# Performance work log

Measured on AMD Instinct MI355X. Metric: run time of the kernel, lower is better.

## Reference

```python
import jax, jax.numpy as jnp
import numpy as np

D_MODEL = 512
EPS = 1e-5


def setup_inputs() -> dict:
    key = jax.random.key(0)
    k1, k2, k3 = jax.random.split(key, 3)
    B, N, D = 8, 2048, D_MODEL
    output = jax.random.normal(k1, (B, N, D), dtype=jnp.float32)
    # multiplicative 0/1 float mask over the [B, N, N] score matrix
    slf_attn_mask = jax.random.randint(k2, (B, N, N), 0, 2).astype(jnp.float32)
    # nn.Linear(d_model, d_model): weight [out, in], xavier-uniform; bias zeros-ish
    limit = float(np.sqrt(6.0 / (D + D)))
    W = jax.random.uniform(k3, (D, D), dtype=jnp.float32, minval=-limit, maxval=limit)
    b = jnp.zeros((D,), dtype=jnp.float32)
    return {"output": output, "slf_attn_mask": slf_attn_mask, "W": W, "b": b}


def reference(output, slf_attn_mask, W, b):
    temperature = jnp.asarray(D_MODEL, output.dtype) ** 0.5
    # scores: [B, N, N] = (q / temp) @ k^T, then multiplicative mask
    attn = jnp.einsum("bnd,bmd->bnm", output / temperature, output) * slf_attn_mask
    # F.normalize(p=2, dim=-1, eps=1e-5): x / max(||x||_2, eps)
    norm = jnp.sqrt(jnp.sum(attn * attn, axis=-1, keepdims=True))
    attn = attn / jnp.maximum(norm, EPS)
    # values: elu(Linear(output)), Linear uses W @ x + b with W [out, in]
    v = jax.nn.elu(jnp.einsum("bnd,ed->bne", output, W) + b)
    return jnp.einsum("bnm,bme->bne", attn, v)
```

## Files before the change

### kernel.cpp

```cpp
#include <hip/hip_runtime.h>
#include <hip/hip_bf16.h>

#define NSEQ 2048
#define DM 512
#define BATCH 8
#define GTOT (BATCH * NSEQ)
#define INV_T 0.044194173824159216f
#define EPSN 1e-5f

typedef __bf16 bf16_t;
typedef bf16_t bf16x8 __attribute__((ext_vector_type(8)));
typedef float f32x4 __attribute__((ext_vector_type(4)));
typedef unsigned short u16;
typedef unsigned int u32;

__device__ __forceinline__ u16 f2bf(float f) {
    u32 u = __builtin_bit_cast(u32, f);
    u32 r = (u + 0x7FFFu + ((u >> 16) & 1u)) >> 16;
    return (u16)r;
}

__global__ __launch_bounds__(256) void k_convert(
    const float* __restrict__ X, const float* __restrict__ W,
    u16* __restrict__ Kbf, u16* __restrict__ Wbf) {
    const long NK = (long)GTOT * DM / 4;
    const long NW = (long)DM * DM / 4;
    long i = (long)blockIdx.x * 256 + threadIdx.x;
    if (i < NK) {
        float4 f = ((const float4*)X)[i];
        ushort4 o;
        o.x = f2bf(f.x); o.y = f2bf(f.y); o.z = f2bf(f.z); o.w = f2bf(f.w);
        ((ushort4*)Kbf)[i] = o;
    } else if (i < NK + NW) {
        long j = i - NK;
        float4 f = ((const float4*)W)[j];
        ushort4 o;
        o.x = f2bf(f.x); o.y = f2bf(f.y); o.z = f2bf(f.z); o.w = f2bf(f.w);
        ((ushort4*)Wbf)[j] = o;
    }
}

__global__ __launch_bounds__(256, 2) void k_vgemm(
    const u16* __restrict__ Wbf, const u16* __restrict__ Kbf,
    const float* __restrict__ bias, u16* __restrict__ vT) {
    __shared__ __attribute__((aligned(16))) u16 Ks[32 * 520];
    const int tid = threadIdx.x;
    const int wave = tid >> 6, lane = tid & 63, quad = lane >> 4, l15 = lane & 15;
    const int etile = blockIdx.x & 7;
    const int mblk = blockIdx.x >> 3;
    const int ebase = etile * 64 + wave * 16;

    bf16x8 wf[16];
    {
        const u16* wp = Wbf + (long)(ebase + l15) * DM + quad * 8;
#pragma unroll
        for (int ks = 0; ks < 16; ++ks) wf[ks] = *(const bf16x8*)(wp + ks * 32);
    }
    float bvals[4];
#pragma unroll
    for (int r = 0; r < 4; ++r) bvals[r] = bias[ebase + quad * 4 + r];

    bf16x8 kreg[8];
    {
        const int g0 = mblk * 256;
#pragma unroll
        for (int j = 0; j < 8; ++j) {
            int c = tid + 256 * j;
            int row = c >> 6, col = c & 63;
            kreg[j] = *(const bf16x8*)(Kbf + (long)(g0 + row) * DM + col * 8);
        }
    }
    for (int mt = 0; mt < 8; ++mt) {
        const int g0 = mblk * 256 + mt * 32;
        __syncthreads();
#pragma unroll
        for (int j = 0; j < 8; ++j) {
            int c = tid + 256 * j;
            int row = c >> 6, col = c & 63;
            *(bf16x8*)(&Ks[row * 520 + col * 8]) = kreg[j];
        }
        __syncthreads();
        {
            int mtn = (mt + 1 < 8) ? mt + 1 : 0;
            const int gn = mblk * 256 + mtn * 32;
#pragma unroll
            for (int j = 0; j < 8; ++j) {
                int c = tid + 256 * j;
                int row = c >> 6, col = c & 63;
                kreg[j] = *(const bf16x8*)(Kbf + (long)(gn + row) * DM + col * 8);
            }
        }
        f32x4 acc[2] = {{0.f, 0.f, 0.f, 0.f}, {0.f, 0.f, 0.f, 0.f}};
#pragma unroll
        for (int ks = 0; ks < 16; ++ks) {
#pragma unroll
            for (int nt = 0; nt < 2; ++nt) {
                bf16x8 kf = *(const bf16x8*)(&Ks[(nt * 16 + l15) * 520 + ks * 32 + quad * 8]);
                acc[nt] = __builtin_amdgcn_mfma_f32_16x16x32_bf16(wf[ks], kf, acc[nt], 0, 0, 0);
            }
        }
#pragma unroll
        for (int nt = 0; nt < 2; ++nt) {
#pragma unroll
            for (int r = 0; r < 4; ++r) {
                int e = ebase + quad * 4 + r;
                int g = g0 + nt * 16 + l15;
                float x = acc[nt][r] + bvals[r];
                float v = x > 0.f ? x : (__expf(x) - 1.f);
                vT[(long)e * GTOT + g] = f2bf(v);
            }
        }
    }
}

__global__ __launch_bounds__(256, 1) void k_flash(
    const u16* __restrict__ Kbf, const u16* __restrict__ vT,
    const float* __restrict__ mask, float* __restrict__ Out) {
    __shared__ __attribute__((aligned(16))) u16 KV[512 * 40];
    __shared__ __attribute__((aligned(16))) u16 Sb[4][16 * 40];
    const int tid = threadIdx.x;
    const int wave = tid >> 6, lane = tid & 63, quad = lane >> 4, l15 = lane & 15;
    const int b = blockIdx.x >> 5;
    const int rblk = blockIdx.x & 31;
    const int r0 = rblk * 64 + wave * 16;

    bf16x8 qf[16];
    {
        const u16* qp = Kbf + (long)(b * NSEQ + r0 + l15) * DM + quad * 8;
#pragma unroll
        for (int ks = 0; ks < 16; ++ks) qf[ks] = *(const bf16x8*)(qp + ks * 32);
    }
    f32x4 oacc[32];
#pragma unroll
    for (int i = 0; i < 32; ++i) oacc[i] = (f32x4){0.f, 0.f, 0.f, 0.f};
    float ss[4] = {0.f, 0.f, 0.f, 0.f};

    const float* mrow = mask + (long)(b * NSEQ + r0 + quad * 4) * NSEQ;
    const u16* kbase = Kbf + (long)b * NSEQ * DM;
    const u16* vbase = vT + (long)b * NSEQ;

    bf16x8 kreg[8];
    float mv[8];
#pragma unroll
    for (int j = 0; j < 8; ++j) {
        int c = tid + 256 * j;
        int row = c >> 6, col = c & 63;
        kreg[j] = *(const bf16x8*)(kbase + (long)row * DM + col * 8);
    }
#pragma unroll
    for (int q = 0; q < 8; ++q) {
        int nt = q >> 2, r = q & 3;
        mv[q] = mrow[(long)r * NSEQ + nt * 16 + l15];
    }

    for (int mt = 0; mt < 64; ++mt) {
        const int m0 = mt * 32;
        __syncthreads();
#pragma unroll
        for (int j = 0; j < 8; ++j) {
            int c = tid + 256 * j;
            int row = c >> 6, col = c & 63;
            *(bf16x8*)(&KV[row * 520 + col * 8]) = kreg[j];
        }
        __syncthreads();
        bf16x8 vreg[8];
#pragma unroll
        for (int dh = 0; dh < 2; ++dh) {
            int d = tid + dh * 256;
            const u16* vp = vbase + (long)d * GTOT + m0;
#pragma unroll
            for (int j = 0; j < 4; ++j) vreg[dh * 4 + j] = *(const bf16x8*)(vp + j * 8);
        }
        f32x4 sacc[2] = {{0.f, 0.f, 0.f, 0.f}, {0.f, 0.f, 0.f, 0.f}};
#pragma unroll
        for (int ks = 0; ks < 16; ++ks) {
#pragma unroll
            for (int nt = 0; nt < 2; ++nt) {
                bf16x8 kf = *(const bf16x8*)(&KV[(nt * 16 + l15) * 520 + ks * 32 + quad * 8]);
                sacc[nt] = __builtin_amdgcn_mfma_f32_16x16x32_bf16(qf[ks], kf, sacc[nt], 0, 0, 0);
            }
        }
#pragma unroll
        for (int nt = 0; nt < 2; ++nt) {
#pragma unroll
            for (int r = 0; r < 4; ++r) {
                float s = sacc[nt][r] * mv[nt * 4 + r] * INV_T;
                ss[r] += s * s;
                Sb[wave][(quad * 4 + r) * 40 + nt * 16 + l15] = f2bf(s);
            }
        }
        __syncthreads();
#pragma unroll
        for (int dh = 0; dh < 2; ++dh) {
            int d = tid + dh * 256;
#pragma unroll
            for (int j = 0; j < 4; ++j) *(bf16x8*)(&KV[d * 40 + j * 8]) = vreg[dh * 4 + j];
        }
        {
            int mtn = (mt + 1 < 64) ? mt + 1 : 0;
            const int mn = mtn * 32;
#pragma unroll
            for (int j = 0; j < 8; ++j) {
                int c = tid + 256 * j;
                int row = c >> 6, col = c & 63;
                kreg[j] = *(const bf16x8*)(kbase + (long)(mn + row) * DM + col * 8);
            }
#pragma unroll
            for (int q = 0; q < 8; ++q) {
                int nt = q >> 2, r = q & 3;
                mv[q] = mrow[(long)r * NSEQ + mn + nt * 16 + l15];
            }
        }
        __syncthreads();
        bf16x8 af = *(const bf16x8*)(&Sb[wave][l15 * 40 + quad * 8]);
#pragma unroll
        for (int nt = 0; nt < 32; ++nt) {
            bf16x8 vf = *(const bf16x8*)(&KV[(nt * 16 + l15) * 40 + quad * 8]);
            oacc[nt] = __builtin_amdgcn_mfma_f32_16x16x32_bf16(af, vf, oacc[nt], 0, 0, 0);
        }
    }
#pragma unroll
    for (int r = 0; r < 4; ++r) {
        float v = ss[r];
        v += __shfl_xor(v, 1, 16);
        v += __shfl_xor(v, 2, 16);
        v += __shfl_xor(v, 4, 16);
        v += __shfl_xor(v, 8, 16);
        ss[r] = 1.f / fmaxf(sqrtf(v), EPSN);
    }
    float* op = Out + (long)(b * NSEQ + r0 + quad * 4) * DM + l15;
#pragma unroll
    for (int nt = 0; nt < 32; ++nt) {
#pragma unroll
        for (int r = 0; r < 4; ++r) op[(long)r * DM + nt * 16] = oacc[nt][r] * ss[r];
    }
}

extern "C" void kernel_launch(void* const* d_in, const int* in_sizes, int n_in,
                              void* d_out, int out_size, void* d_ws, size_t ws_size,
                              hipStream_t stream) {
    const float* X = (const float*)d_in[0];
    const float* mask = (const float*)d_in[1];
    const float* W = (const float*)d_in[2];
    const float* bias = (const float*)d_in[3];
    float* out = (float*)d_out;

    char* ws = (char*)d_ws;
    u16* Kbf = (u16*)ws;
    u16* Wbf = (u16*)(ws + 16777216);
    u16* vT = (u16*)(ws + 16777216 + 524288);

    k_convert<<<8448, 256, 0, stream>>>(X, W, Kbf, Wbf);
    k_vgemm<<<512, 256, 0, stream>>>(Wbf, Kbf, bias, vT);
    k_flash<<<256, 256, 0, stream>>>(Kbf, vT, mask, out);
}
```

Baseline: 372.5 us.

## Replace fused flash kernel with separate tiled score and PV GEMMs

Splits the fused attention kernel into an S GEMM that writes masked bf16 scores and accumulates row sum-of-squares via atomics, then a PV GEMM that applies the row normalization. All GEMMs now use 128x128 tiles with 32x32x16 MFMA, async global-to-LDS loads and a swizzled LDS layout, and run at higher occupancy. The fused kernel had only 256 blocks with heavy per-block syncs. The split gains parallelism but materializes a 64MB score matrix in global memory, adding extra traffic and atomics.

After: 354.4 us. 4.8% less time.

```diff
diff --git a/kernel.cpp b/kernel.cpp
--- a/kernel.cpp
+++ b/kernel.cpp
@@ -10,7 +10,7 @@
 
 typedef __bf16 bf16_t;
 typedef bf16_t bf16x8 __attribute__((ext_vector_type(8)));
-typedef float f32x4 __attribute__((ext_vector_type(4)));
+typedef float f32x16 __attribute__((ext_vector_type(16)));
 typedef unsigned short u16;
 typedef unsigned int u32;
 
@@ -20,11 +20,33 @@
     return (u16)r;
 }
 
+__device__ __forceinline__ void async16(const u16* g, u16* l) {
+    __builtin_amdgcn_global_load_lds(
+        (const __attribute__((address_space(1))) u32*)g,
+        (__attribute__((address_space(3))) u32*)l, 16, 0, 0);
+}
+
+__device__ __forceinline__ bf16x8 fragld(const u16* t, int row, int kc) {
+    return *(const bf16x8*)(t + row * 32 + ((kc ^ ((row >> 1) & 3)) << 3));
+}
+
+#define MFMA32(a, b, c) __builtin_amdgcn_mfma_f32_32x32x16_bf16(a, b, c, 0, 0, 0)
+#define ROWOFF(reg, lh) (((reg) & 3) + 8 * ((reg) >> 2) + 4 * (lh))
+
+#define STAGE(Ag, ldA, Bg, ldB, k0)                                              \
+    do {                                                                         \
+        async16((Ag) + (long)rA0 * (ldA) + (k0) + kcg * 8, Ab + u0 * 512 + lane * 8);        \
+        async16((Ag) + (long)(rA0 + 16) * (ldA) + (k0) + kcg * 8, Ab + (u0 + 1) * 512 + lane * 8); \
+        async16((Bg) + (long)rA0 * (ldB) + (k0) + kcg * 8, Bb + u0 * 512 + lane * 8);        \
+        async16((Bg) + (long)(rA0 + 16) * (ldB) + (k0) + kcg * 8, Bb + (u0 + 1) * 512 + lane * 8); \
+    } while (0)
+
 __global__ __launch_bounds__(256) void k_convert(
     const float* __restrict__ X, const float* __restrict__ W,
-    u16* __restrict__ Kbf, u16* __restrict__ Wbf) {
+    u16* __restrict__ Kbf, u16* __restrict__ Wbf, float* __restrict__ ssbuf) {
     const long NK = (long)GTOT * DM / 4;
     const long NW = (long)DM * DM / 4;
+    const long NS = GTOT / 4;
     long i = (long)blockIdx.x * 256 + threadIdx.x;
     if (i < NK) {
         float4 f = ((const float4*)X)[i];
@@ -37,75 +59,62 @@
         ushort4 o;
         o.x = f2bf(f.x); o.y = f2bf(f.y); o.z = f2bf(f.z); o.w = f2bf(f.w);
         ((ushort4*)Wbf)[j] = o;
-    }
-}
-
-__global__ __launch_bounds__(256, 2) void k_vgemm(
+    } else if (i < NK + NW + NS) {
+        ((float4*)ssbuf)[i - NK - NW] = (float4){0.f, 0.f, 0.f, 0.f};
+    }
+}
+
+__global__ __launch_bounds__(256, 4) void k_vgemm(
     const u16* __restrict__ Wbf, const u16* __restrict__ Kbf,
     const float* __restrict__ bias, u16* __restrict__ vT) {
-    __shared__ __attribute__((aligned(16))) u16 Ks[32 * 520];
-    const int tid = threadIdx.x;
-    const int wave = tid >> 6, lane = tid & 63, quad = lane >> 4, l15 = lane & 15;
-    const int etile = blockIdx.x & 7;
-    const int mblk = blockIdx.x >> 3;
-    const int ebase = etile * 64 + wave * 16;
-
-    bf16x8 wf[16];
-    {
-        const u16* wp = Wbf + (long)(ebase + l15) * DM + quad * 8;
-#pragma unroll
-        for (int ks = 0; ks < 16; ++ks) wf[ks] = *(const bf16x8*)(wp + ks * 32);
-    }
-    float bvals[4];
-#pragma unroll
-    for (int r = 0; r < 4; ++r) bvals[r] = bias[ebase + quad * 4 + r];
-
-    bf16x8 kreg[8];
-    {
-        const int g0 = mblk * 256;
-#pragma unroll
-        for (int j = 0; j < 8; ++j) {
-            int c = tid + 256 * j;
-            int row = c >> 6, col = c & 63;
-            kreg[j] = *(const bf16x8*)(Kbf + (long)(g0 + row) * DM + col * 8);
-        }
-    }
-    for (int mt = 0; mt < 8; ++mt) {
-        const int g0 = mblk * 256 + mt * 32;
-        __syncthreads();
-#pragma unroll
-        for (int j = 0; j < 8; ++j) {
-            int c = tid + 256 * j;
-            int row = c >> 6, col = c & 63;
-            *(bf16x8*)(&Ks[row * 520 + col * 8]) = kreg[j];
-        }
-        __syncthreads();
-        {
-            int mtn = (mt + 1 < 8) ? mt + 1 : 0;
-            const int gn = mblk * 256 + mtn * 32;
-#pragma unroll
-            for (int j = 0; j < 8; ++j) {
-                int c = tid + 256 * j;
-                int row = c >> 6, col = c & 63;
-                kreg[j] = *(const bf16x8*)(Kbf + (long)(gn + row) * DM + col * 8);
-            }
-        }
-        f32x4 acc[2] = {{0.f, 0.f, 0.f, 0.f}, {0.f, 0.f, 0.f, 0.f}};
-#pragma unroll
-        for (int ks = 0; ks < 16; ++ks) {
-#pragma unroll
-            for (int nt = 0; nt < 2; ++nt) {
-                bf16x8 kf = *(const bf16x8*)(&Ks[(nt * 16 + l15) * 520 + ks * 32 + quad * 8]);
-                acc[nt] = __builtin_amdgcn_mfma_f32_16x16x32_bf16(wf[ks], kf, acc[nt], 0, 0, 0);
-            }
-        }
-#pragma unroll
-        for (int nt = 0; nt < 2; ++nt) {
-#pragma unroll
-            for (int r = 0; r < 4; ++r) {
-                int e = ebase + quad * 4 + r;
-                int g = g0 + nt * 16 + l15;
-                float x = acc[nt][r] + bvals[r];
+    __shared__ __attribute__((aligned(16))) u16 Ab[4096], Bb[4096];
+    const int tid = threadIdx.x, wave = tid >> 6, lane = tid & 63;
+    const int l31 = lane & 31, lh = lane >> 5;
+    const int wy = wave >> 1, wx = wave & 1;
+    const int M0 = blockIdx.y * 128, N0 = blockIdx.x * 128;
+    const u16* Ag = Wbf + (long)M0 * DM;
+    const u16* Bg = Kbf + (long)N0 * DM;
+
+    const int u0 = wave * 2;
+    const int rA0 = u0 * 16 + (lane >> 2);
+    const int kcg = (lane & 3) ^ ((lane >> 3) & 3);
+
+    f32x16 acc[2][2];
+#pragma unroll
+    for (int i = 0; i < 2; ++i)
+#pragma unroll
+        for (int j = 0; j < 2; ++j)
+#pragma unroll
+            for (int e = 0; e < 16; ++e) acc[i][j][e] = 0.f;
+
+    for (int kt = 0; kt < 16; ++kt) {
+        const int k0 = kt * 32;
+        __syncthreads();
+        STAGE(Ag, DM, Bg, DM, k0);
+        __syncthreads();
+#pragma unroll
+        for (int ks = 0; ks < 2; ++ks) {
+            int kc = ks * 2 + lh;
+            bf16x8 a0 = fragld(Ab, wy * 64 + l31, kc);
+            bf16x8 a1 = fragld(Ab, wy * 64 + 32 + l31, kc);
+            bf16x8 b0 = fragld(Bb, wx * 64 + l31, kc);
+            bf16x8 b1 = fragld(Bb, wx * 64 + 32 + l31, kc);
+            acc[0][0] = MFMA32(a0, b0, acc[0][0]);
+            acc[0][1] = MFMA32(a0, b1, acc[0][1]);
+            acc[1][0] = MFMA32(a1, b0, acc[1][0]);
+            acc[1][1] = MFMA32(a1, b1, acc[1][1]);
+        }
+    }
+#pragma unroll
+    for (int mi = 0; mi < 2; ++mi) {
+#pragma unroll
+        for (int reg = 0; reg < 16; ++reg) {
+            int e = M0 + wy * 64 + mi * 32 + ROWOFF(reg, lh);
+            float bv = bias[e];
+#pragma unroll
+            for (int ni = 0; ni < 2; ++ni) {
+                int g = N0 + wx * 64 + ni * 32 + l31;
+                float x = acc[mi][ni][reg] + bv;
                 float v = x > 0.f ? x : (__expf(x) - 1.f);
                 vT[(long)e * GTOT + g] = f2bf(v);
             }
@@ -113,126 +122,132 @@
     }
 }
 
-__global__ __launch_bounds__(256, 1) void k_flash(
-    const u16* __restrict__ Kbf, const u16* __restrict__ vT,
-    const float* __restrict__ mask, float* __restrict__ Out) {
-    __shared__ __attribute__((aligned(16))) u16 KV[512 * 40];
-    __shared__ __attribute__((aligned(16))) u16 Sb[4][16 * 40];
-    const int tid = threadIdx.x;
-    const int wave = tid >> 6, lane = tid & 63, quad = lane >> 4, l15 = lane & 15;
-    const int b = blockIdx.x >> 5;
-    const int rblk = blockIdx.x & 31;
-    const int r0 = rblk * 64 + wave * 16;
-
-    bf16x8 qf[16];
-    {
-        const u16* qp = Kbf + (long)(b * NSEQ + r0 + l15) * DM + quad * 8;
-#pragma unroll
-        for (int ks = 0; ks < 16; ++ks) qf[ks] = *(const bf16x8*)(qp + ks * 32);
-    }
-    f32x4 oacc[32];
-#pragma unroll
-    for (int i = 0; i < 32; ++i) oacc[i] = (f32x4){0.f, 0.f, 0.f, 0.f};
-    float ss[4] = {0.f, 0.f, 0.f, 0.f};
-
-    const float* mrow = mask + (long)(b * NSEQ + r0 + quad * 4) * NSEQ;
-    const u16* kbase = Kbf + (long)b * NSEQ * DM;
-    const u16* vbase = vT + (long)b * NSEQ;
-
-    bf16x8 kreg[8];
-    float mv[8];
-#pragma unroll
-    for (int j = 0; j < 8; ++j) {
-        int c = tid + 256 * j;
-        int row = c >> 6, col = c & 63;
-        kreg[j] = *(const bf16x8*)(kbase + (long)row * DM + col * 8);
-    }
-#pragma unroll
-    for (int q = 0; q < 8; ++q) {
-        int nt = q >> 2, r = q & 3;
-        mv[q] = mrow[(long)r * NSEQ + nt * 16 + l15];
-    }
-
-    for (int mt = 0; mt < 64; ++mt) {
-        const int m0 = mt * 32;
-        __syncthreads();
-#pragma unroll
-        for (int j = 0; j < 8; ++j) {
-            int c = tid + 256 * j;
-            int row = c >> 6, col = c & 63;
-            *(bf16x8*)(&KV[row * 520 + col * 8]) = kreg[j];
-        }
-        __syncthreads();
-        bf16x8 vreg[8];
-#pragma unroll
-        for (int dh = 0; dh < 2; ++dh) {
-            int d = tid + dh * 256;
-            const u16* vp = vbase + (long)d * GTOT + m0;
-#pragma unroll
-            for (int j = 0; j < 4; ++j) vreg[dh * 4 + j] = *(const bf16x8*)(vp + j * 8);
-        }
-        f32x4 sacc[2] = {{0.f, 0.f, 0.f, 0.f}, {0.f, 0.f, 0.f, 0.f}};
-#pragma unroll
-        for (int ks = 0; ks < 16; ++ks) {
-#pragma unroll
-            for (int nt = 0; nt < 2; ++nt) {
-                bf16x8 kf = *(const bf16x8*)(&KV[(nt * 16 + l15) * 520 + ks * 32 + quad * 8]);
-                sacc[nt] = __builtin_amdgcn_mfma_f32_16x16x32_bf16(qf[ks], kf, sacc[nt], 0, 0, 0);
+__global__ __launch_bounds__(256, 4) void k_sgemm(
+    const u16* __restrict__ Kbf, const float* __restrict__ mask,
+    u16* __restrict__ Sbuf, float* __restrict__ ssbuf) {
+    __shared__ __attribute__((aligned(16))) u16 Ab[4096], Bb[4096];
+    const int tid = threadIdx.x, wave = tid >> 6, lane = tid & 63;
+    const int l31 = lane & 31, lh = lane >> 5;
+    const int wy = wave >> 1, wx = wave & 1;
+    const int b = blockIdx.z;
+    const int M0 = blockIdx.y * 128, N0 = blockIdx.x * 128;
+    const u16* Ag = Kbf + (long)(b * NSEQ + M0) * DM;
+    const u16* Bg = Kbf + (long)(b * NSEQ + N0) * DM;
+
+    const int u0 = wave * 2;
+    const int rA0 = u0 * 16 + (lane >> 2);
+    const int kcg = (lane & 3) ^ ((lane >> 3) & 3);
+
+    f32x16 acc[2][2];
+#pragma unroll
+    for (int i = 0; i < 2; ++i)
+#pragma unroll
+        for (int j = 0; j < 2; ++j)
+#pragma unroll
+            for (int e = 0; e < 16; ++e) acc[i][j][e] = 0.f;
+
+    for (int kt = 0; kt < 16; ++kt) {
+        const int k0 = kt * 32;
+        __syncthreads();
+        STAGE(Ag, DM, Bg, DM, k0);
+        __syncthreads();
+#pragma unroll
+        for (int ks = 0; ks < 2; ++ks) {
+            int kc = ks * 2 + lh;
+            bf16x8 a0 = fragld(Ab, wy * 64 + l31, kc);
+            bf16x8 a1 = fragld(Ab, wy * 64 + 32 + l31, kc);
+            bf16x8 b0 = fragld(Bb, wx * 64 + l31, kc);
+            bf16x8 b1 = fragld(Bb, wx * 64 + 32 + l31, kc);
+            acc[0][0] = MFMA32(a0, b0, acc[0][0]);
+            acc[0][1] = MFMA32(a0, b1, acc[0][1]);
+            acc[1][0] = MFMA32(a1, b0, acc[1][0]);
+            acc[1][1] = MFMA32(a1, b1, acc[1][1]);
+        }
+    }
+#pragma unroll
+    for (int mi = 0; mi < 2; ++mi) {
+#pragma unroll
+        for (int reg = 0; reg < 16; ++reg) {
+            long rg = (long)b * NSEQ + M0 + wy * 64 + mi * 32 + ROWOFF(reg, lh);
+            float v = 0.f;
+#pragma unroll
+            for (int ni = 0; ni < 2; ++ni) {
+                int cg = N0 + wx * 64 + ni * 32 + l31;
+                float s = acc[mi][ni][reg] * INV_T * mask[rg * NSEQ + cg];
+                v += s * s;
+                Sbuf[rg * NSEQ + cg] = f2bf(s);
             }
-        }
-#pragma unroll
-        for (int nt = 0; nt < 2; ++nt) {
-#pragma unroll
-            for (int r = 0; r < 4; ++r) {
-                float s = sacc[nt][r] * mv[nt * 4 + r] * INV_T;
-                ss[r] += s * s;
-                Sb[wave][(quad * 4 + r) * 40 + nt * 16 + l15] = f2bf(s);
+            v += __shfl_xor(v, 1, 32);
+            v += __shfl_xor(v, 2, 32);
+            v += __shfl_xor(v, 4, 32);
+            v += __shfl_xor(v, 8, 32);
+            v += __shfl_xor(v, 16, 32);
+            if (l31 == 0) atomicAdd(&ssbuf[rg], v);
+        }
+    }
+}
+
+__global__ __launch_bounds__(256, 4) void k_pv(
+    const u16* __restrict__ Sbuf, const u16* __restrict__ vT,
+    const float* __restrict__ ssbuf, float* __restrict__ Out) {
+    __shared__ __attribute__((aligned(16))) u16 Ab[4096], Bb[4096];
+    __shared__ float sc[128];
+    const int tid = threadIdx.x, wave = tid >> 6, lane = tid & 63;
+    const int l31 = lane & 31, lh = lane >> 5;
+    const int wy = wave >> 1, wx = wave & 1;
+    const int b = blockIdx.z;
+    const int M0 = blockIdx.y * 128, N0 = blockIdx.x * 128;
+    const u16* Ag = Sbuf + (long)(b * NSEQ + M0) * NSEQ;
+    const u16* Bg = vT + (long)N0 * GTOT + b * NSEQ;
+
+    if (tid < 128) {
+        float v = ssbuf[b * NSEQ + M0 + tid];
+        sc[tid] = 1.f / fmaxf(sqrtf(v), EPSN);
+    }
+
+    const int u0 = wave * 2;
+    const int rA0 = u0 * 16 + (lane >> 2);
+    const int kcg = (lane & 3) ^ ((lane >> 3) & 3);
+
+    f32x16 acc[2][2];
+#pragma unroll
+    for (int i = 0; i < 2; ++i)
+#pragma unroll
+        for (int j = 0; j < 2; ++j)
+#pragma unroll
+            for (int e = 0; e < 16; ++e) acc[i][j][e] = 0.f;
+
+    for (int kt = 0; kt < 64; ++kt) {
+        const int k0 = kt * 32;
+        __syncthreads();
+        STAGE(Ag, NSEQ, Bg, GTOT, k0);
+        __syncthreads();
+#pragma unroll
+        for (int ks = 0; ks < 2; ++ks) {
+            int kc = ks * 2 + lh;
+            bf16x8 a0 = fragld(Ab, wy * 64 + l31, kc);
+            bf16x8 a1 = fragld(Ab, wy * 64 + 32 + l31, kc);
+            bf16x8 b0 = fragld(Bb, wx * 64 + l31, kc);
+            bf16x8 b1 = fragld(Bb, wx * 64 + 32 + l31, kc);
+            acc[0][0] = MFMA32(a0, b0, acc[0][0]);
+            acc[0][1] = MFMA32(a0, b1, acc[0][1]);
+            acc[1][0] = MFMA32(a1, b0, acc[1][0]);
+            acc[1][1] = MFMA32(a1, b1, acc[1][1]);
+        }
+    }
+#pragma unroll
+    for (int mi = 0; mi < 2; ++mi) {
+#pragma unroll
+        for (int reg = 0; reg < 16; ++reg) {
+            int rl = wy * 64 + mi * 32 + ROWOFF(reg, lh);
+            float s = sc[rl];
+            float* op = Out + ((long)b * NSEQ + M0 + rl) * DM;
+#pragma unroll
+            for (int ni = 0; ni < 2; ++ni) {
+                int d = N0 + wx * 64 + ni * 32 + l31;
+                op[d] = acc[mi][ni][reg] * s;
             }
         }
-        __syncthreads();
-#pragma unroll
-        for (int dh = 0; dh < 2; ++dh) {
-            int d = tid + dh * 256;
-#pragma unroll
-            for (int j = 0; j < 4; ++j) *(bf16x8*)(&KV[d * 40 + j * 8]) = vreg[dh * 4 + j];
-        }
-        {
-            int mtn = (mt + 1 < 64) ? mt + 1 : 0;
-            const int mn = mtn * 32;
-#pragma unroll
-            for (int j = 0; j < 8; ++j) {
-                int c = tid + 256 * j;
-                int row = c >> 6, col = c & 63;
-                kreg[j] = *(const bf16x8*)(kbase + (long)(mn + row) * DM + col * 8);
-            }
-#pragma unroll
-            for (int q = 0; q < 8; ++q) {
-                int nt = q >> 2, r = q & 3;
-                mv[q] = mrow[(long)r * NSEQ + mn + nt * 16 + l15];
-            }
-        }
-        __syncthreads();
-        bf16x8 af = *(const bf16x8*)(&Sb[wave][l15 * 40 + quad * 8]);
-#pragma unroll
-        for (int nt = 0; nt < 32; ++nt) {
-            bf16x8 vf = *(const bf16x8*)(&KV[(nt * 16 + l15) * 40 + quad * 8]);
-            oacc[nt] = __builtin_amdgcn_mfma_f32_16x16x32_bf16(af, vf, oacc[nt], 0, 0, 0);
-        }
-    }
-#pragma unroll
-    for (int r = 0; r < 4; ++r) {
-        float v = ss[r];
-        v += __shfl_xor(v, 1, 16);
-        v += __shfl_xor(v, 2, 16);
-        v += __shfl_xor(v, 4, 16);
-        v += __shfl_xor(v, 8, 16);
-        ss[r] = 1.f / fmaxf(sqrtf(v), EPSN);
-    }
-    float* op = Out + (long)(b * NSEQ + r0 + quad * 4) * DM + l15;
-#pragma unroll
-    for (int nt = 0; nt < 32; ++nt) {
-#pragma unroll
-        for (int r = 0; r < 4; ++r) op[(long)r * DM + nt * 16] = oacc[nt][r] * ss[r];
     }
 }
 
@@ -248,9 +263,12 @@
     char* ws = (char*)d_ws;
     u16* Kbf = (u16*)ws;
     u16* Wbf = (u16*)(ws + 16777216);
-    u16* vT = (u16*)(ws + 16777216 + 524288);
-
-    k_convert<<<8448, 256, 0, stream>>>(X, W, Kbf, Wbf);
-    k_vgemm<<<512, 256, 0, stream>>>(Wbf, Kbf, bias, vT);
-    k_flash<<<256, 256, 0, stream>>>(Kbf, vT, mask, out);
-}
+    u16* vT = (u16*)(ws + 17301504);
+    u16* Sbuf = (u16*)(ws + 34078720);
+    float* ssbuf = (float*)(ws + 101187584);
+
+    k_convert<<<8464, 256, 0, stream>>>(X, W, Kbf, Wbf, ssbuf);
+    k_vgemm<<<dim3(128, 4), 256, 0, stream>>>(Wbf, Kbf, bias, vT);
+    k_sgemm<<<dim3(16, 16, 8), 256, 0, stream>>>(Kbf, mask, Sbuf, ssbuf);
+    k_pv<<<dim3(4, 16, 8), 256, 0, stream>>>(Sbuf, vT, ssbuf, out);
+}
```
